# Optimization experiments

Hardware: AMD Instinct MI355X
Metric: run time of the kernel (lower is better)

## Reference

```python
import jax, jax.numpy as jnp
import numpy as np
import math

SUN = 9.0            # global SuN constant in the repo (sudoku N=9)
TB = 16              # t-block size for L1-score computation (bounds peak memory)


def quick_gelu(x):
    return x * jax.nn.sigmoid(1.702 * x)


def l1_scores(q, k):
    # q, k: (b, t, h, d)  ->  scores (b, h, t, s) = -sum_d |q[b,t,h,:] - k[b,s,h,:]|
    # Blocked over t so we never materialize the full (b,t,s,h,d) tensor.
    b, t, h, d = q.shape
    nb = t // TB
    qb = q.reshape(b, nb, TB, h, d).swapaxes(0, 1)  # (nb, b, TB, h, d)

    def blk(carry, qi):
        # qi: (b, TB, h, d); diff block: (b, TB, s, h, d) -> (b, TB, s, h)
        s = -jnp.sum(jnp.abs(qi[:, :, None, :, :] - k[:, None, :, :, :]), axis=-1)
        return carry, s

    _, out = jax.lax.scan(blk, None, qb)            # (nb, b, TB, s, h)
    out = out.transpose(1, 0, 2, 3, 4).reshape(b, t, t, h)  # (b, t, s, h)
    return out.transpose(0, 3, 1, 2)                # (b, h, t, s)


def setup_inputs() -> dict:
    key = jax.random.key(0)
    ks = jax.random.split(key, 5)
    b, t, d, h = 8, 512, 128, 8
    x = jax.random.normal(ks[0], (b, t, d), dtype=jnp.float32)
    msk = jax.random.uniform(ks[1], (1, h, t, t), dtype=jnp.float32)
    # LinearM(d_model, n_head*2*d_model): w is (outdim, indim+1), uniform*scl, bias col zeroed
    scl_qv = math.sqrt(6.0) / math.sqrt(d + h * 2 * d)
    wqv_w = jax.random.uniform(ks[2], (h * 2 * d, d + 1), dtype=jnp.float32) * scl_qv
    wqv_w = wqv_w.at[:, -1].set(0.0)
    # LinearNobias(d_model, n_head): w is (n_head, d_model); used directly as per-head k-gate
    scl_k = math.sqrt(6.0) / math.sqrt(d + h)
    wk_w = jax.random.uniform(ks[3], (h, d), dtype=jnp.float32) * scl_k
    # fanout = LinearM(d_model, d_model)
    scl_f = math.sqrt(6.0) / math.sqrt(2 * d)
    fanout_w = jax.random.uniform(ks[4], (d, d + 1), dtype=jnp.float32) * scl_f
    fanout_w = fanout_w.at[:, -1].set(0.0)
    return {"x": x, "msk": msk, "wqv_w": wqv_w, "wk_w": wk_w, "fanout_w": fanout_w}


def reference(x, msk, wqv_w, wk_w, fanout_w):
    b, t, d = x.shape
    h = wk_w.shape[0]
    # wqv: LinearM -> (b, t, h*2*d)
    y = jnp.einsum('oi,bti->bto', wqv_w[:, :-1], x) + wqv_w[:, -1]
    y = y.reshape(b, t, h, 2 * d)
    q, v = y[..., :d], y[..., d:]                      # each (b, t, h, d)
    # k = x expanded per head, gated elementwise by wk.w (per-head, per-dim gate)
    k = x[:, :, None, :] * wk_w[None, None, :, :]      # (b, t, h, d)
    # gv gate: all heads enabled (init_zeros=False) -> identity multiply on v
    a = l1_scores(q, k) / math.sqrt(d)                 # (b, h, t, s)
    a = jax.nn.softmax(a, axis=3) * msk                # mask AFTER softmax (as in source)
    # combine + sum over heads: einsum('bhts,bshd->bthd') then sum(dim=2 of bthd == h)
    bo = jnp.einsum('bhts,bshd->btd', a, v)            # (b, t, d)
    yo = quick_gelu(bo + SUN / 2.0) - SUN / 2.0
    yo = jnp.einsum('oi,bti->bto', fanout_w[:, :-1], yo) + fanout_w[:, -1]
    return x + yo
```

## Files before the change

kernel.cpp:

```cpp
#include <hip/hip_runtime.h>
#include <hip/hip_bf16.h>
#include <math.h>

#define BB 8
#define TT 512
#define DD 128
#define HH 8
#define OO 2048
#define WCOLS 129
#define SCALE 0.08838834764831845f
#define IT 16
#define SC2 64
#define NC (TT / SC2)
#define Q8SCL 32.0f
#define Q8OFF 128.0f
#define SCALE_Q8 (SCALE / Q8SCL)

typedef __attribute__((ext_vector_type(8))) short short8;
typedef __attribute__((ext_vector_type(4))) float floatx4;

static __device__ __forceinline__ float bf2f(__hip_bfloat16 v) { return __bfloat162float(v); }
static __device__ __forceinline__ float us2f(unsigned short u) {
  union { unsigned int i; float f; } cv; cv.i = ((unsigned int)u) << 16; return cv.f;
}
static __device__ __forceinline__ unsigned short f2us(float f) {
  union { float f; unsigned int i; } cv; cv.f = f;
  unsigned int lsb = (cv.i >> 16) & 1u;
  return (unsigned short)((cv.i + 0x7fffu + lsb) >> 16);
}
static __device__ __forceinline__ float ldin(const void* p, int i, int isf) {
  return isf ? ((const float*)p)[i] : bf2f(((const __hip_bfloat16*)p)[i]);
}
static __device__ __forceinline__ unsigned char quant8(float v) {
  float f = fminf(fmaxf(v * Q8SCL + Q8OFF, 0.0f), 255.0f);
  return (unsigned char)(f + 0.5f);
}
static __device__ __forceinline__ int detect_isf(const void* x) {
  const unsigned int* w = (const unsigned int*)x;
  int cnt = 0;
#pragma unroll
  for (int i = 0; i < 64; ++i) {
    float a = fabsf(us2f((unsigned short)(w[i] & 0xFFFFu)));
    cnt += (a > 0.05f && a < 8.0f) ? 1 : 0;
  }
  return (cnt < 32) ? 1 : 0;
}

#if __has_builtin(__builtin_amdgcn_sad_u8)
#define SAD8(a, b, c) __builtin_amdgcn_sad_u8((a), (b), (c))
#elif __has_builtin(__builtin_amdgcn_sad_u16)
static __device__ __forceinline__ unsigned int SAD8(unsigned int a, unsigned int b, unsigned int c) {
  unsigned int alo = a & 0x00FF00FFu, ahi = (a >> 8) & 0x00FF00FFu;
  unsigned int blo = b & 0x00FF00FFu, bhi = (b >> 8) & 0x00FF00FFu;
  c = __builtin_amdgcn_sad_u16(alo, blo, c);
  return __builtin_amdgcn_sad_u16(ahi, bhi, c);
}
#else
static __device__ __forceinline__ unsigned int SAD8(unsigned int a, unsigned int b, unsigned int c) {
#pragma unroll
  for (int i = 0; i < 4; ++i) {
    int d = (int)((a >> (8 * i)) & 0xFF) - (int)((b >> (8 * i)) & 0xFF);
    c += (unsigned int)(d < 0 ? -d : d);
  }
  return c;
}
#endif

__global__ void k_prep(const void* __restrict__ x,
                       const void* __restrict__ wqv,
                       const void* __restrict__ wk,
                       const void* __restrict__ fo,
                       float* __restrict__ qvb,
                       float* __restrict__ foT, float* __restrict__ fob,
                       float* __restrict__ wkf,
                       unsigned short* __restrict__ wqvb,
                       unsigned short* __restrict__ xb,
                       int* __restrict__ flg) {
  int isf = detect_isf(x);
  int stride = gridDim.x * blockDim.x;
  int idx = blockIdx.x * blockDim.x + threadIdx.x;
  if (idx == 0) *flg = isf;
  for (int i = idx; i < OO * DD; i += stride) {
    int o = i >> 7, ii = i & 127;
    wqvb[i] = f2us(ldin(wqv, o * WCOLS + ii, isf));
  }
  for (int o = idx; o < OO; o += stride) qvb[o] = ldin(wqv, o * WCOLS + DD, isf);
  for (int i = idx; i < DD * DD; i += stride) {
    int o = i & (DD - 1), ii = i >> 7;
    foT[i] = ldin(fo, o * WCOLS + ii, isf);
  }
  for (int o = idx; o < DD; o += stride) fob[o] = ldin(fo, o * WCOLS + DD, isf);
  for (int i = idx; i < HH * DD; i += stride) wkf[i] = ldin(wk, i, isf);
  for (int i = idx; i < BB * TT * DD; i += stride) xb[i] = f2us(ldin(x, i, isf));
}

__global__ __launch_bounds__(256) void k_qvm(const unsigned short* __restrict__ xb,
                                             const unsigned short* __restrict__ wqvb,
                                             const float* __restrict__ qvb,
                                             unsigned char* __restrict__ q2b,
                                             unsigned short* __restrict__ vt) {
  __shared__ __align__(16) unsigned short xs[32][136];
  __shared__ __align__(16) unsigned short vtile[128][40];
  int rb = blockIdx.x * 32;
  int cb = blockIdx.y * 256;
  int tid = threadIdx.x;
#pragma unroll
  for (int p = 0; p < 2; ++p) {
    int e = tid + p * 256;
    int row = e >> 4, c16 = e & 15;
    *(uint4*)&xs[row][c16 * 8] = *(const uint4*)&xb[(size_t)(rb + row) * DD + c16 * 8];
  }
  __syncthreads();
  int lane = tid & 63;
  int w = tid >> 6;
  int mI = lane & 15;
  int quad = lane >> 4;
  int cw = cb + w * 64;
  floatx4 acc[2][4];
#pragma unroll
  for (int rt = 0; rt < 2; ++rt)
#pragma unroll
    for (int ct = 0; ct < 4; ++ct) acc[rt][ct] = (floatx4){0.f, 0.f, 0.f, 0.f};
#pragma unroll
  for (int j = 0; j < 4; ++j) {
    short8 av[2], bv[4];
#pragma unroll
    for (int rt = 0; rt < 2; ++rt)
      av[rt] = *(const short8*)&xs[rt * 16 + mI][j * 32 + quad * 8];
#pragma unroll
    for (int ct = 0; ct < 4; ++ct)
      bv[ct] = *(const short8*)&wqvb[(size_t)(cw + ct * 16 + mI) * DD + j * 32 + quad * 8];
#pragma unroll
    for (int rt = 0; rt < 2; ++rt)
#pragma unroll
      for (int ct = 0; ct < 4; ++ct)
        acc[rt][ct] = __builtin_amdgcn_mfma_f32_16x16x32_bf16(av[rt], bv[ct], acc[rt][ct], 0, 0, 0);
  }
#pragma unroll
  for (int rt = 0; rt < 2; ++rt) {
#pragma unroll
    for (int ct = 0; ct < 4; ++ct) {
      int o = cw + ct * 16 + mI;
      float bias = qvb[o];
      int h = o >> 8, cc = o & 255;
#pragma unroll
      for (int reg = 0; reg < 4; ++reg) {
        int r = rb + rt * 16 + quad * 4 + reg;
        int b = r >> 9, t = r & 511;
        float val = acc[rt][ct][reg] + bias;
        if (cc < DD) {
          size_t base = ((size_t)(b * HH + h) * TT + t) * DD;
          q2b[base + cc] = quant8(val);
        } else {
          vtile[cc - DD][r - rb] = f2us(val);
        }
      }
    }
  }
  __syncthreads();
  {
    int b = rb >> 9, t0 = rb & 511;
    int h = cb >> 8;
    int n = tid >> 1, half = tid & 1;
    unsigned short* dst = vt + (((size_t)(b * HH + h) * DD) + n) * TT + t0 + half * 16;
    uint4 a0 = *(const uint4*)&vtile[n][half * 16];
    uint4 a1 = *(const uint4*)&vtile[n][half * 16 + 8];
    *(uint4*)&dst[0] = a0;
    *(uint4*)&dst[8] = a1;
  }
}

__global__ void k_k(const unsigned short* __restrict__ xb,
                    const float* __restrict__ wkf, unsigned char* __restrict__ ku8) {
  int idx = blockIdx.x * 256 + threadIdx.x;
  int d = idx & 127;
  int s = (idx >> 7) & 511;
  int h = (idx >> 16) & 7;
  int b = idx >> 19;
  float val = us2f(xb[(b * TT + s) * DD + d]) * wkf[h * DD + d];
  ku8[idx] = quant8(val);
}

__global__ __launch_bounds__(256) void k_flash(const void* __restrict__ msk,
                                               const int* __restrict__ flag,
                                               const unsigned char* __restrict__ q2b,
                                               const unsigned char* __restrict__ ku8,
                                               const unsigned short* __restrict__ vt,
                                               unsigned short* __restrict__ yo8) {
  __shared__ __align__(16) unsigned int qp[IT][36];
  __shared__ __align__(16) unsigned int kp[2][SC2][36];
  __shared__ __align__(16) unsigned short ps[IT][TT + 8];
  int isf = *flag;
  int bh = blockIdx.x;
  int h = bh & 7;
  int it0 = blockIdx.y * IT;
  int tid = threadIdx.x;

  const uint4* qrow = (const uint4*)(q2b + ((size_t)bh * TT + it0) * DD);
  if (tid < 128) {
    *(uint4*)&qp[tid >> 3][(tid & 7) * 4] = qrow[tid];
  }

  int ig2 = tid >> 5;
  int si = tid & 31;
  int r0 = ig2 * 2, r1 = r0 + 1;
  int rot = (si & 7) * 4;
  float r[32];

  const uint4* kc4 = (const uint4*)(ku8 + (size_t)bh * TT * DD);
  uint4 kreg[2];
#pragma unroll
  for (int p = 0; p < 2; ++p) kreg[p] = kc4[tid + p * 256];

#pragma unroll
  for (int c = 0; c < NC; ++c) {
    unsigned int (*kb)[36] = kp[c & 1];
#pragma unroll
    for (int p = 0; p < 2; ++p) {
      int e = tid + p * 256;
      *(uint4*)&kb[e >> 3][(e & 7) * 4] = kreg[p];
    }
    if (c < NC - 1) {
#pragma unroll
      for (int p = 0; p < 2; ++p)
        kreg[p] = kc4[(c + 1) * 512 + tid + p * 256];
    }
    __syncthreads();
    unsigned int a00 = 0, a01 = 0, a10 = 0, a11 = 0;
    const unsigned int* k0r = &kb[2 * si][0];
    const unsigned int* k1r = &kb[2 * si + 1][0];
    const unsigned int* q0r = &qp[r0][0];
    const unsigned int* q1r = &qp[r1][0];
#pragma unroll
    for (int j8 = 0; j8 < 32; j8 += 8) {
      int i0 = (j8 + rot) & 31;
      int i1 = (j8 + rot + 4) & 31;
      uint4 qa0 = *(const uint4*)&q0r[i0];
      uint4 qa1 = *(const uint4*)&q0r[i1];
      uint4 qb0 = *(const uint4*)&q1r[i0];
      uint4 qb1 = *(const uint4*)&q1r[i1];
      uint4 ka0 = *(const uint4*)&k0r[i0];
      uint4 ka1 = *(const uint4*)&k0r[i1];
      uint4 kb0 = *(const uint4*)&k1r[i0];
      uint4 kb1 = *(const uint4*)&k1r[i1];
      a00 = SAD8(qa0.x, ka0.x, a00); a00 = SAD8(qa0.y, ka0.y, a00);
      a00 = SAD8(qa0.z, ka0.z, a00); a00 = SAD8(qa0.w, ka0.w, a00);
      a00 = SAD8(qa1.x, ka1.x, a00); a00 = SAD8(qa1.y, ka1.y, a00);
      a00 = SAD8(qa1.z, ka1.z, a00); a00 = SAD8(qa1.w, ka1.w, a00);
      a01 = SAD8(qa0.x, kb0.x, a01); a01 = SAD8(qa0.y, kb0.y, a01);
      a01 = SAD8(qa0.z, kb0.z, a01); a01 = SAD8(qa0.w, kb0.w, a01);
      a01 = SAD8(qa1.x, kb1.x, a01); a01 = SAD8(qa1.y, kb1.y, a01);
      a01 = SAD8(qa1.z, kb1.z, a01); a01 = SAD8(qa1.w, kb1.w, a01);
      a10 = SAD8(qb0.x, ka0.x, a10); a10 = SAD8(qb0.y, ka0.y, a10);
      a10 = SAD8(qb0.z, ka0.z, a10); a10 = SAD8(qb0.w, ka0.w, a10);
      a10 = SAD8(qb1.x, ka1.x, a10); a10 = SAD8(qb1.y, ka1.y, a10);
      a10 = SAD8(qb1.z, ka1.z, a10); a10 = SAD8(qb1.w, ka1.w, a10);
      a11 = SAD8(qb0.x, kb0.x, a11); a11 = SAD8(qb0.y, kb0.y, a11);
      a11 = SAD8(qb0.z, kb0.z, a11); a11 = SAD8(qb0.w, kb0.w, a11);
      a11 = SAD8(qb1.x, kb1.x, a11); a11 = SAD8(qb1.y, kb1.y, a11);
      a11 = SAD8(qb1.z, kb1.z, a11); a11 = SAD8(qb1.w, kb1.w, a11);
    }
    r[c * 2]          = -(float)a00 * SCALE_Q8;
    r[c * 2 + 1]      = -(float)a01 * SCALE_Q8;
    r[16 + c * 2]     = -(float)a10 * SCALE_Q8;
    r[16 + c * 2 + 1] = -(float)a11 * SCALE_Q8;
  }

  float m0 = -1e30f, m1 = -1e30f;
#pragma unroll
  for (int j = 0; j < 16; ++j) { m0 = fmaxf(m0, r[j]); m1 = fmaxf(m1, r[16 + j]); }
#pragma unroll
  for (int off = 16; off; off >>= 1) {
    m0 = fmaxf(m0, __shfl_xor(m0, off, 32));
    m1 = fmaxf(m1, __shfl_xor(m1, off, 32));
  }
  float s0 = 0.f, s1 = 0.f;
#pragma unroll
  for (int j = 0; j < 16; ++j) {
    r[j] = __expf(r[j] - m0);           s0 += r[j];
    r[16 + j] = __expf(r[16 + j] - m1); s1 += r[16 + j];
  }
#pragma unroll
  for (int off = 16; off; off >>= 1) {
    s0 += __shfl_xor(s0, off, 32);
    s1 += __shfl_xor(s1, off, 32);
  }
  float inv0 = 1.0f / s0, inv1 = 1.0f / s1;

  int mb0 = (h * TT + it0 + r0) * TT;
  int mb1 = mb0 + TT;
#pragma unroll
  for (int c = 0; c < NC; ++c) {
    int s = c * SC2 + 2 * si;
    float p00 = r[c * 2]          * inv0 * ldin(msk, mb0 + s, isf);
    float p01 = r[c * 2 + 1]      * inv0 * ldin(msk, mb0 + s + 1, isf);
    float p10 = r[16 + c * 2]     * inv1 * ldin(msk, mb1 + s, isf);
    float p11 = r[16 + c * 2 + 1] * inv1 * ldin(msk, mb1 + s + 1, isf);
    *(unsigned int*)&ps[r0][s] = (unsigned int)f2us(p00) | ((unsigned int)f2us(p01) << 16);
    *(unsigned int*)&ps[r1][s] = (unsigned int)f2us(p10) | ((unsigned int)f2us(p11) << 16);
  }
  __syncthreads();

  {
    int lane = tid & 63;
    int w = tid >> 6;
    int mI = lane & 15;
    int quad = lane >> 4;
    int n0 = w * 32;
    floatx4 acc0 = {0.f, 0.f, 0.f, 0.f};
    floatx4 acc1 = {0.f, 0.f, 0.f, 0.f};
    const unsigned short* vb0 = vt + ((size_t)bh * DD + n0 + mI) * TT;
    const unsigned short* vb1 = vb0 + 16 * TT;
#pragma unroll
    for (int st = 0; st < 4; ++st) {
      short8 av[4], b0v[4], b1v[4];
#pragma unroll
      for (int j = 0; j < 4; ++j) {
        int krow = st * 128 + j * 32 + quad * 8;
        b0v[j] = *(const short8*)&vb0[krow];
        b1v[j] = *(const short8*)&vb1[krow];
        av[j]  = *(const short8*)&ps[mI][krow];
      }
#pragma unroll
      for (int j = 0; j < 4; ++j) {
        acc0 = __builtin_amdgcn_mfma_f32_16x16x32_bf16(av[j], b0v[j], acc0, 0, 0, 0);
        acc1 = __builtin_amdgcn_mfma_f32_16x16x32_bf16(av[j], b1v[j], acc1, 0, 0, 0);
      }
    }
    unsigned short* yb = yo8 + ((size_t)bh * TT + it0) * DD;
#pragma unroll
    for (int reg = 0; reg < 4; ++reg) {
      int row = quad * 4 + reg;
      yb[row * DD + n0 + mI]      = f2us(acc0[reg]);
      yb[row * DD + n0 + 16 + mI] = f2us(acc1[reg]);
    }
  }
}

__global__ __launch_bounds__(256) void k_fanout(const void* __restrict__ x,
                                                const int* __restrict__ flag,
                                                const unsigned short* __restrict__ yo8,
                                                const float* __restrict__ foT,
                                                const float* __restrict__ fob,
                                                void* __restrict__ outv) {
  __shared__ float ys[16][132];
  int isf = *flag;
  int m0 = blockIdx.x * 16;
  int tid = threadIdx.x;
#pragma unroll
  for (int p = 0; p < 8; ++p) {
    int e = tid + p * 256;
    int mr = e >> 7, ii = e & 127;
    int r = m0 + mr;
    int bb = r >> 9, t = r & 511;
    size_t base = ((size_t)bb * HH * TT + t) * DD + ii;
    float sacc = 0.f;
#pragma unroll
    for (int hh = 0; hh < HH; ++hh) sacc += us2f(yo8[base + (size_t)hh * TT * DD]);
    float z = sacc + 4.5f;
    ys[mr][ii] = z / (1.0f + __expf(-1.702f * z)) - 4.5f;
  }
  __syncthreads();
  int ty = tid >> 5, tx = tid & 31;
  float acc[2][4] = {};
  for (int ii = 0; ii < 128; ++ii) {
    float4 w4 = *(const float4*)(foT + ii * DD + tx * 4);
    float y0 = ys[ty * 2 + 0][ii], y1 = ys[ty * 2 + 1][ii];
    acc[0][0] += y0 * w4.x; acc[0][1] += y0 * w4.y; acc[0][2] += y0 * w4.z; acc[0][3] += y0 * w4.w;
    acc[1][0] += y1 * w4.x; acc[1][1] += y1 * w4.y; acc[1][2] += y1 * w4.z; acc[1][3] += y1 * w4.w;
  }
#pragma unroll
  for (int rr = 0; rr < 2; ++rr) {
    int r = m0 + ty * 2 + rr;
#pragma unroll
    for (int c = 0; c < 4; ++c) {
      int o = tx * 4 + c;
      float val = acc[rr][c] + fob[o] + ldin(x, r * DD + o, isf);
      if (isf) ((float*)outv)[r * DD + o] = val;
      else     ((__hip_bfloat16*)outv)[r * DD + o] = __float2bfloat16(val);
    }
  }
}

extern "C" void kernel_launch(void* const* d_in, const int* in_sizes, int n_in,
                              void* d_out, int out_size, void* d_ws, size_t ws_size,
                              hipStream_t stream) {
  const void* x   = d_in[0];
  const void* msk = d_in[1];
  const void* wqv = d_in[2];
  const void* wk  = d_in[3];
  const void* fo  = d_in[4];

  float* qvb = (float*)d_ws;
  float* foT = qvb + 2048;
  float* fob = foT + 16384;
  float* wkf = fob + 128;
  int*   flg = (int*)(wkf + 1024);
  unsigned short* wqvb = (unsigned short*)(flg + 16);
  unsigned short* xb   = wqvb + 262144;
  unsigned char*  q2b  = (unsigned char*)(xb + 524288);
  unsigned char*  ku8  = q2b + 4194304;
  unsigned short* v2   = (unsigned short*)(ku8 + 4194304);
  unsigned short* vt   = v2 + 4194304;
  unsigned short* yo8  = v2;

  k_prep<<<256, 256, 0, stream>>>(x, wqv, wk, fo, qvb, foT, fob, wkf, wqvb, xb, flg);
  k_qvm<<<dim3(128, 8), 256, 0, stream>>>(xb, wqvb, qvb, q2b, vt);
  k_k<<<16384, 256, 0, stream>>>(xb, wkf, ku8);
  k_flash<<<dim3(64, 32), 256, 0, stream>>>(msk, flg, q2b, ku8, vt, yo8);
  k_fanout<<<256, 256, 0, stream>>>(x, flg, yo8, foT, fob, d_out);
}
```

Baseline: 177.7 us.

## Vectorize conversions, stage q tile in LDS, alias flash smem buffers

Converts x to bf16 with float4 loads and packed stores, and passes bf16 input through unchanged. In k_qvm the quantized q values are staged in shared memory so they go out as coalesced 16-byte row writes instead of scattered byte stores. In k_flash the k double buffer is unrolled by two and its second buffer shares memory with the probability tile, which lowers LDS use and may raise occupancy, at the cost of an extra barrier. k_fanout now reads the per-head outputs with 8-wide vector loads.

```diff
diff --git a/kernel.cpp b/kernel.cpp
--- a/kernel.cpp
+++ b/kernel.cpp
@@ -91,7 +91,20 @@
   }
   for (int o = idx; o < DD; o += stride) fob[o] = ldin(fo, o * WCOLS + DD, isf);
   for (int i = idx; i < HH * DD; i += stride) wkf[i] = ldin(wk, i, isf);
-  for (int i = idx; i < BB * TT * DD; i += stride) xb[i] = f2us(ldin(x, i, isf));
+  {
+    int n4 = BB * TT * DD / 4;
+    for (int i4 = idx; i4 < n4; i4 += stride) {
+      if (isf) {
+        float4 f = ((const float4*)x)[i4];
+        unsigned int lo = (unsigned int)f2us(f.x) | ((unsigned int)f2us(f.y) << 16);
+        unsigned int hi = (unsigned int)f2us(f.z) | ((unsigned int)f2us(f.w) << 16);
+        uint2 o2; o2.x = lo; o2.y = hi;
+        ((uint2*)xb)[i4] = o2;
+      } else {
+        ((uint2*)xb)[i4] = ((const uint2*)x)[i4];
+      }
+    }
+  }
 }
 
 __global__ __launch_bounds__(256) void k_qvm(const unsigned short* __restrict__ xb,
@@ -101,6 +114,7 @@
                                              unsigned short* __restrict__ vt) {
   __shared__ __align__(16) unsigned short xs[32][136];
   __shared__ __align__(16) unsigned short vtile[128][40];
+  __shared__ __align__(16) unsigned char qtile[32][144];
   int rb = blockIdx.x * 32;
   int cb = blockIdx.y * 256;
   int tid = threadIdx.x;
@@ -142,18 +156,13 @@
     for (int ct = 0; ct < 4; ++ct) {
       int o = cw + ct * 16 + mI;
       float bias = qvb[o];
-      int h = o >> 8, cc = o & 255;
+      int cc = o & 255;
 #pragma unroll
       for (int reg = 0; reg < 4; ++reg) {
         int r = rb + rt * 16 + quad * 4 + reg;
-        int b = r >> 9, t = r & 511;
         float val = acc[rt][ct][reg] + bias;
-        if (cc < DD) {
-          size_t base = ((size_t)(b * HH + h) * TT + t) * DD;
-          q2b[base + cc] = quant8(val);
-        } else {
-          vtile[cc - DD][r - rb] = f2us(val);
-        }
+        if (cc < DD) qtile[r - rb][cc] = quant8(val);
+        else         vtile[cc - DD][r - rb] = f2us(val);
       }
     }
   }
@@ -161,12 +170,19 @@
   {
     int b = rb >> 9, t0 = rb & 511;
     int h = cb >> 8;
-    int n = tid >> 1, half = tid & 1;
-    unsigned short* dst = vt + (((size_t)(b * HH + h) * DD) + n) * TT + t0 + half * 16;
-    uint4 a0 = *(const uint4*)&vtile[n][half * 16];
-    uint4 a1 = *(const uint4*)&vtile[n][half * 16 + 8];
-    *(uint4*)&dst[0] = a0;
-    *(uint4*)&dst[8] = a1;
+    {
+      int row = tid >> 3, c16 = (tid & 7) * 16;
+      unsigned char* qdst = q2b + ((size_t)(b * HH + h) * TT + t0 + row) * DD + c16;
+      *(uint4*)qdst = *(const uint4*)&qtile[row][c16];
+    }
+    {
+      int n = tid >> 1, half = tid & 1;
+      unsigned short* dst = vt + (((size_t)(b * HH + h) * DD) + n) * TT + t0 + half * 16;
+      uint4 a0 = *(const uint4*)&vtile[n][half * 16];
+      uint4 a1 = *(const uint4*)&vtile[n][half * 16 + 8];
+      *(uint4*)&dst[0] = a0;
+      *(uint4*)&dst[8] = a1;
+    }
   }
 }
 
@@ -181,15 +197,61 @@
   ku8[idx] = quant8(val);
 }
 
+static __device__ __forceinline__ void sad_chunk(const unsigned int (*__restrict__ kb)[36],
+                                                 const unsigned int (*__restrict__ qp)[36],
+                                                 int r0, int r1, int si, int rot,
+                                                 float* __restrict__ r, int c) {
+  unsigned int a00 = 0, a01 = 0, a10 = 0, a11 = 0;
+  const unsigned int* k0r = &kb[2 * si][0];
+  const unsigned int* k1r = &kb[2 * si + 1][0];
+  const unsigned int* q0r = &qp[r0][0];
+  const unsigned int* q1r = &qp[r1][0];
+#pragma unroll
+  for (int j8 = 0; j8 < 32; j8 += 8) {
+    int i0 = (j8 + rot) & 31;
+    int i1 = (j8 + rot + 4) & 31;
+    uint4 qa0 = *(const uint4*)&q0r[i0];
+    uint4 qa1 = *(const uint4*)&q0r[i1];
+    uint4 qb0 = *(const uint4*)&q1r[i0];
+    uint4 qb1 = *(const uint4*)&q1r[i1];
+    uint4 ka0 = *(const uint4*)&k0r[i0];
+    uint4 ka1 = *(const uint4*)&k0r[i1];
+    uint4 kb0 = *(const uint4*)&k1r[i0];
+    uint4 kb1 = *(const uint4*)&k1r[i1];
+    a00 = SAD8(qa0.x, ka0.x, a00); a00 = SAD8(qa0.y, ka0.y, a00);
+    a00 = SAD8(qa0.z, ka0.z, a00); a00 = SAD8(qa0.w, ka0.w, a00);
+    a00 = SAD8(qa1.x, ka1.x, a00); a00 = SAD8(qa1.y, ka1.y, a00);
+    a00 = SAD8(qa1.z, ka1.z, a00); a00 = SAD8(qa1.w, ka1.w, a00);
+    a01 = SAD8(qa0.x, kb0.x, a01); a01 = SAD8(qa0.y, kb0.y, a01);
+    a01 = SAD8(qa0.z, kb0.z, a01); a01 = SAD8(qa0.w, kb0.w, a01);
+    a01 = SAD8(qa1.x, kb1.x, a01); a01 = SAD8(qa1.y, kb1.y, a01);
+    a01 = SAD8(qa1.z, kb1.z, a01); a01 = SAD8(qa1.w, kb1.w, a01);
+    a10 = SAD8(qb0.x, ka0.x, a10); a10 = SAD8(qb0.y, ka0.y, a10);
+    a10 = SAD8(qb0.z, ka0.z, a10); a10 = SAD8(qb0.w, ka0.w, a10);
+    a10 = SAD8(qb1.x, ka1.x, a10); a10 = SAD8(qb1.y, ka1.y, a10);
+    a10 = SAD8(qb1.z, ka1.z, a10); a10 = SAD8(qb1.w, ka1.w, a10);
+    a11 = SAD8(qb0.x, kb0.x, a11); a11 = SAD8(qb0.y, kb0.y, a11);
+    a11 = SAD8(qb0.z, kb0.z, a11); a11 = SAD8(qb0.w, kb0.w, a11);
+    a11 = SAD8(qb1.x, kb1.x, a11); a11 = SAD8(qb1.y, kb1.y, a11);
+    a11 = SAD8(qb1.z, kb1.z, a11); a11 = SAD8(qb1.w, kb1.w, a11);
+  }
+  r[c * 2]          = -(float)a00 * SCALE_Q8;
+  r[c * 2 + 1]      = -(float)a01 * SCALE_Q8;
+  r[16 + c * 2]     = -(float)a10 * SCALE_Q8;
+  r[16 + c * 2 + 1] = -(float)a11 * SCALE_Q8;
+}
+
 __global__ __launch_bounds__(256) void k_flash(const void* __restrict__ msk,
                                                const int* __restrict__ flag,
                                                const unsigned char* __restrict__ q2b,
                                                const unsigned char* __restrict__ ku8,
                                                const unsigned short* __restrict__ vt,
                                                unsigned short* __restrict__ yo8) {
-  __shared__ __align__(16) unsigned int qp[IT][36];
-  __shared__ __align__(16) unsigned int kp[2][SC2][36];
-  __shared__ __align__(16) unsigned short ps[IT][TT + 8];
+  __shared__ __align__(16) unsigned char smem[2304 + 9216 + 16640];
+  unsigned int (*qp)[36]  = (unsigned int (*)[36])smem;
+  unsigned int (*kpA)[36] = (unsigned int (*)[36])(smem + 2304);
+  unsigned int (*kpB)[36] = (unsigned int (*)[36])(smem + 11520);
+  unsigned short (*ps)[TT + 8] = (unsigned short (*)[TT + 8])(smem + 11520);
   int isf = *flag;
   int bh = blockIdx.x;
   int h = bh & 7;
@@ -213,57 +275,29 @@
   for (int p = 0; p < 2; ++p) kreg[p] = kc4[tid + p * 256];
 
 #pragma unroll
-  for (int c = 0; c < NC; ++c) {
-    unsigned int (*kb)[36] = kp[c & 1];
+  for (int cc = 0; cc < NC; cc += 2) {
 #pragma unroll
     for (int p = 0; p < 2; ++p) {
       int e = tid + p * 256;
-      *(uint4*)&kb[e >> 3][(e & 7) * 4] = kreg[p];
-    }
-    if (c < NC - 1) {
+      *(uint4*)&kpA[e >> 3][(e & 7) * 4] = kreg[p];
+    }
+#pragma unroll
+    for (int p = 0; p < 2; ++p)
+      kreg[p] = kc4[(cc + 1) * 512 + tid + p * 256];
+    __syncthreads();
+    sad_chunk(kpA, qp, r0, r1, si, rot, r, cc);
+#pragma unroll
+    for (int p = 0; p < 2; ++p) {
+      int e = tid + p * 256;
+      *(uint4*)&kpB[e >> 3][(e & 7) * 4] = kreg[p];
+    }
+    if (cc + 2 < NC) {
 #pragma unroll
       for (int p = 0; p < 2; ++p)
-        kreg[p] = kc4[(c + 1) * 512 + tid + p * 256];
+        kreg[p] = kc4[(cc + 2) * 512 + tid + p * 256];
     }
     __syncthreads();
-    unsigned int a00 = 0, a01 = 0, a10 = 0, a11 = 0;
-    const unsigned int* k0r = &kb[2 * si][0];
-    const unsigned int* k1r = &kb[2 * si + 1][0];
-    const unsigned int* q0r = &qp[r0][0];
-    const unsigned int* q1r = &qp[r1][0];
-#pragma unroll
-    for (int j8 = 0; j8 < 32; j8 += 8) {
-      int i0 = (j8 + rot) & 31;
-      int i1 = (j8 + rot + 4) & 31;
-      uint4 qa0 = *(const uint4*)&q0r[i0];
-      uint4 qa1 = *(const uint4*)&q0r[i1];
-      uint4 qb0 = *(const uint4*)&q1r[i0];
-      uint4 qb1 = *(const uint4*)&q1r[i1];
-      uint4 ka0 = *(const uint4*)&k0r[i0];
-      uint4 ka1 = *(const uint4*)&k0r[i1];
-      uint4 kb0 = *(const uint4*)&k1r[i0];
-      uint4 kb1 = *(const uint4*)&k1r[i1];
-      a00 = SAD8(qa0.x, ka0.x, a00); a00 = SAD8(qa0.y, ka0.y, a00);
-      a00 = SAD8(qa0.z, ka0.z, a00); a00 = SAD8(qa0.w, ka0.w, a00);
-      a00 = SAD8(qa1.x, ka1.x, a00); a00 = SAD8(qa1.y, ka1.y, a00);
-      a00 = SAD8(qa1.z, ka1.z, a00); a00 = SAD8(qa1.w, ka1.w, a00);
-      a01 = SAD8(qa0.x, kb0.x, a01); a01 = SAD8(qa0.y, kb0.y, a01);
-      a01 = SAD8(qa0.z, kb0.z, a01); a01 = SAD8(qa0.w, kb0.w, a01);
-      a01 = SAD8(qa1.x, kb1.x, a01); a01 = SAD8(qa1.y, kb1.y, a01);
-      a01 = SAD8(qa1.z, kb1.z, a01); a01 = SAD8(qa1.w, kb1.w, a01);
-      a10 = SAD8(qb0.x, ka0.x, a10); a10 = SAD8(qb0.y, ka0.y, a10);
-      a10 = SAD8(qb0.z, ka0.z, a10); a10 = SAD8(qb0.w, ka0.w, a10);
-      a10 = SAD8(qb1.x, ka1.x, a10); a10 = SAD8(qb1.y, ka1.y, a10);
-      a10 = SAD8(qb1.z, ka1.z, a10); a10 = SAD8(qb1.w, ka1.w, a10);
-      a11 = SAD8(qb0.x, kb0.x, a11); a11 = SAD8(qb0.y, kb0.y, a11);
-      a11 = SAD8(qb0.z, kb0.z, a11); a11 = SAD8(qb0.w, kb0.w, a11);
-      a11 = SAD8(qb1.x, kb1.x, a11); a11 = SAD8(qb1.y, kb1.y, a11);
-      a11 = SAD8(qb1.z, kb1.z, a11); a11 = SAD8(qb1.w, kb1.w, a11);
-    }
-    r[c * 2]          = -(float)a00 * SCALE_Q8;
-    r[c * 2 + 1]      = -(float)a01 * SCALE_Q8;
-    r[16 + c * 2]     = -(float)a10 * SCALE_Q8;
-    r[16 + c * 2 + 1] = -(float)a11 * SCALE_Q8;
+    sad_chunk(kpB, qp, r0, r1, si, rot, r, cc + 1);
   }
 
   float m0 = -1e30f, m1 = -1e30f;
@@ -286,6 +320,8 @@
     s1 += __shfl_xor(s1, off, 32);
   }
   float inv0 = 1.0f / s0, inv1 = 1.0f / s1;
+
+  __syncthreads();
 
   int mb0 = (h * TT + it0 + r0) * TT;
   int mb1 = mb0 + TT;
@@ -347,18 +383,24 @@
   int isf = *flag;
   int m0 = blockIdx.x * 16;
   int tid = threadIdx.x;
-#pragma unroll
-  for (int p = 0; p < 8; ++p) {
-    int e = tid + p * 256;
-    int mr = e >> 7, ii = e & 127;
+  {
+    int mr = tid >> 4;
+    int i8 = (tid & 15) * 8;
     int r = m0 + mr;
     int bb = r >> 9, t = r & 511;
-    size_t base = ((size_t)bb * HH * TT + t) * DD + ii;
-    float sacc = 0.f;
-#pragma unroll
-    for (int hh = 0; hh < HH; ++hh) sacc += us2f(yo8[base + (size_t)hh * TT * DD]);
-    float z = sacc + 4.5f;
-    ys[mr][ii] = z / (1.0f + __expf(-1.702f * z)) - 4.5f;
+    size_t base = ((size_t)bb * HH * TT + t) * DD + i8;
+    float s[8] = {0.f, 0.f, 0.f, 0.f, 0.f, 0.f, 0.f, 0.f};
+#pragma unroll
+    for (int hh = 0; hh < HH; ++hh) {
+      short8 v = *(const short8*)&yo8[base + (size_t)hh * TT * DD];
+#pragma unroll
+      for (int j = 0; j < 8; ++j) s[j] += us2f((unsigned short)v[j]);
+    }
+#pragma unroll
+    for (int j = 0; j < 8; ++j) {
+      float z = s[j] + 4.5f;
+      ys[mr][i8 + j] = z / (1.0f + __expf(-1.702f * z)) - 4.5f;
+    }
   }
   __syncthreads();
   int ty = tid >> 5, tx = tid & 31;
```

Measured after the change: 184.3 us. 3.7% more time.
